# Optimization experiments

Measured on AMD Instinct MI355X. Metric: run time of the kernel, lower is better.

## Reference

```python
import jax, jax.numpy as jnp
import numpy as np

K = 3          # deformable conv kernel size
PAD = 1        # padding
BN_EPS = 1e-5


def _upsample2(x):
    # nn.Upsample(scale_factor=2) default mode='nearest' on [B,C,D,H,W]
    x = jnp.repeat(x, 2, axis=2)
    x = jnp.repeat(x, 2, axis=3)
    x = jnp.repeat(x, 2, axis=4)
    return x


def _conv3d(x, w, b):
    out = jax.lax.conv_general_dilated(
        x, w, window_strides=(1, 1, 1), padding=[(PAD, PAD)] * 3,
        dimension_numbers=('NCDHW', 'OIDHW', 'NCDHW'))
    return out + b[None, :, None, None, None]


def _trilinear_sample(x, coords):
    # x: [B,C,D,H,W]; coords: [B,Kt,3,D,H,W] absolute (possibly OOB) positions.
    # Zero padding outside the volume (standard deformable-conv convention).
    B, C, D, H, W = x.shape
    pd, ph, pw = coords[:, :, 0], coords[:, :, 1], coords[:, :, 2]  # [B,Kt,D,H,W]
    d0 = jnp.floor(pd); h0 = jnp.floor(ph); w0 = jnp.floor(pw)
    fd = pd - d0; fh = ph - h0; fw = pw - w0
    x_flat = x.reshape(B, C, D * H * W)

    def gather(di, hi, wi):
        valid = ((di >= 0) & (di < D) & (hi >= 0) & (hi < H) & (wi >= 0) & (wi < W))
        dc = jnp.clip(di, 0, D - 1).astype(jnp.int32)
        hc = jnp.clip(hi, 0, H - 1).astype(jnp.int32)
        wc = jnp.clip(wi, 0, W - 1).astype(jnp.int32)
        flat = (dc * H + hc) * W + wc                       # [B,Kt,D,H,W]
        vals = jax.vmap(lambda xf, idx: jnp.take(xf, idx.reshape(-1), axis=1))(x_flat, flat)
        vals = vals.reshape(B, C, *flat.shape[1:])          # [B,C,Kt,D,H,W]
        return vals * valid[:, None].astype(x.dtype)

    out = jnp.zeros((B, C) + pd.shape[1:], x.dtype)
    for dd in (0, 1):
        for hh in (0, 1):
            for ww in (0, 1):
                wgt = ((fd if dd else 1.0 - fd)
                       * (fh if hh else 1.0 - fh)
                       * (fw if ww else 1.0 - fw))           # [B,Kt,D,H,W]
                out = out + gather(d0 + dd, h0 + hh, w0 + ww) * wgt[:, None]
    return out  # [B,C,Kt,D,H,W]


def _deform_conv3d(x, w_off, b_off, w, b):
    B, C, D, H, W = x.shape
    Kt = K ** 3
    # offsets: Conv3d(C, 3*K^3, k=3, pad=1) -> [B, Kt, 3(dz,dy,dx), D,H,W]
    off = _conv3d(x, w_off, b_off).reshape(B, Kt, 3, D, H, W)
    # kernel tap displacements relative to output voxel: [Kt,3]
    taps = jnp.stack(jnp.meshgrid(jnp.arange(K), jnp.arange(K), jnp.arange(K),
                                  indexing='ij'), -1).reshape(-1, 3).astype(x.dtype) - PAD
    grid = jnp.stack(jnp.meshgrid(jnp.arange(D, dtype=x.dtype),
                                  jnp.arange(H, dtype=x.dtype),
                                  jnp.arange(W, dtype=x.dtype),
                                  indexing='ij'), 0)          # [3,D,H,W]
    coords = grid[None, None] + taps[None, :, :, None, None, None] + off  # [B,Kt,3,D,H,W]
    sampled = _trilinear_sample(x, coords)                    # [B,C,Kt,D,H,W]
    out = jnp.einsum('bckdhw,ock->bodhw', sampled, w.reshape(w.shape[0], C, Kt))
    return out + b[None, :, None, None, None]


def setup_inputs() -> dict:
    key = jax.random.key(0)
    ks = jax.random.split(key, 4)
    ch_in, ch_out = 64, 32
    x = jax.random.normal(ks[0], (1, ch_in, 16, 16, 16), jnp.float32)
    w_off = jax.random.normal(ks[1], (3 * K ** 3, ch_in, K, K, K), jnp.float32) * 0.01
    b_off = jnp.zeros((3 * K ** 3,), jnp.float32)
    w = jax.random.normal(ks[2], (ch_out, ch_in, K, K, K), jnp.float32) * 0.05
    b = jnp.zeros((ch_out,), jnp.float32)
    gamma = jnp.ones((ch_out,), jnp.float32)
    beta = jnp.zeros((ch_out,), jnp.float32)
    return {"x": x, "w_off": w_off, "b_off": b_off, "w": w, "b": b,
            "gamma": gamma, "beta": beta}


def reference(x, w_off, b_off, w, b, gamma, beta):
    x = _upsample2(x)                                  # [B,C,2D,2H,2W]
    out = _deform_conv3d(x, w_off, b_off, w, b)        # [B,ch_out,2D,2H,2W]
    # BatchNorm3d (training-mode batch stats) + ReLU
    mean = out.mean(axis=(0, 2, 3, 4), keepdims=True)
    var = out.var(axis=(0, 2, 3, 4), keepdims=True)
    out = (out - mean) * jax.lax.rsqrt(var + BN_EPS)
    out = out * gamma[None, :, None, None, None] + beta[None, :, None, None, None]
    return jax.nn.relu(out)
```

## Files before the change

kernel.cpp:

```cpp
#include <hip/hip_runtime.h>
#include <math.h>

#define NVOX  32768
#define CIN   64
#define COUT  32
#define KT    27
#define CIT   1728
#define PSP   5832

#define WS_XT   0
#define WS_WA   186624
#define WS_W2   214272
#define WS_STAT 410880
#define WS_P    410944

typedef __attribute__((ext_vector_type(8))) _Float16 half8;
typedef __attribute__((ext_vector_type(2))) _Float16 half2v;
typedef __attribute__((ext_vector_type(4))) float floatx4;

static __device__ __forceinline__ unsigned dup16(float w) {
    unsigned short b = __builtin_bit_cast(unsigned short, (_Float16)w);
    return (unsigned)b * 0x10001u;
}
static __device__ __forceinline__ half2v u2h2(unsigned u) {
    return __builtin_bit_cast(half2v, u);
}
static __device__ __forceinline__ half8 pk8(half2v a, half2v b, half2v c, half2v d) {
    union { half8 v; half2v p[4]; } u;
    u.p[0] = a; u.p[1] = b; u.p[2] = c; u.p[3] = d;
    return u.v;
}

__global__ __launch_bounds__(256) void prep_all_kernel(
        const float* __restrict__ x, const float* __restrict__ w_off,
        const float* __restrict__ wmat, float* __restrict__ ws) {
    int b = blockIdx.x, t = threadIdx.x;
    if (b < 92) {
        __shared__ _Float16 tile[64][65];
        _Float16* xth = (_Float16*)(ws + WS_XT);
        int tq = t >> 6, lane = t & 63;
        int base = b * 64;
        int cell = base + lane;
        int qw = cell % 18, qh = (cell / 18) % 18, qd = cell / 324;
        bool interior = (cell < PSP) && qd >= 1 && qd <= 16 && qh >= 1 && qh <= 16
                        && qw >= 1 && qw <= 16;
        int xbase = interior ? (((qd - 1) * 16 + (qh - 1)) * 16 + (qw - 1)) : 0;
#pragma unroll
        for (int i = 0; i < 16; i++) {
            int c = tq * 16 + i;
            float v = interior ? x[c * 4096 + xbase] : 0.f;
            tile[lane][c] = (_Float16)v;
        }
        __syncthreads();
#pragma unroll
        for (int i = 0; i < 16; i++) {
            int s = tq * 16 + i;
            int cell2 = base + s;
            if (cell2 < PSP) xth[cell2 * 64 + lane] = tile[s][lane];
        }
    } else if (b < 119) {
        _Float16* wa = (_Float16*)(ws + WS_WA);
        int idx = (b - 92) * 256 + t;
        int kb = idx >> 5, o = idx & 31;
        half8 r;
#pragma unroll
        for (int j = 0; j < 8; j++) {
            int kk = kb * 8 + j;
            int tap = kk >> 6, ci = kk & 63;
            r[j] = (_Float16)wmat[o * CIT + ci * 27 + tap];
        }
        *(half8*)(wa + idx * 8) = r;
    } else if (b < 311) {
        _Float16* w2 = (_Float16*)(ws + WS_W2);
        int idx = (b - 119) * 256 + t;
        int pi = idx / 6144;
        int rem = idx - pi * 6144;
        int kb = rem / 96, m = rem - (rem / 96) * 96;
        int pid = pi >> 2, pih = (pi >> 1) & 1, piw = pi & 1;
        half8 r;
#pragma unroll
        for (int j = 0; j < 8; j++) {
            int kk = kb * 8 + j;
            int tap2 = kk >> 6, ci = kk & 63;
            int cd = tap2 >> 2, ch = (tap2 >> 1) & 1, cw = tap2 & 1;
            int bd = pid ? (cd ? 2 : 0) : cd;
            int nd = pid ? (cd ? 1 : 2) : (cd ? 2 : 1);
            int bh = pih ? (ch ? 2 : 0) : ch;
            int nh = pih ? (ch ? 1 : 2) : (ch ? 2 : 1);
            int bw = piw ? (cw ? 2 : 0) : cw;
            int nw = piw ? (cw ? 1 : 2) : (cw ? 2 : 1);
            float s = 0.f;
            if (m < 81) {
                const float* wp = w_off + (m * 64 + ci) * 27;
                for (int a = 0; a < nd; a++)
                    for (int bb = 0; bb < nh; bb++)
                        for (int c = 0; c < nw; c++)
                            s += wp[(bd + a) * 9 + (bh + bb) * 3 + (bw + c)];
            }
            r[j] = (_Float16)s;
        }
        *(half8*)(w2 + idx * 8) = r;
    } else {
        if (t < 64) ws[WS_STAT + t] = 0.f;
    }
}

__global__ __launch_bounds__(256, 4) void offset_kernel(
        const float* __restrict__ b_off, float* ws) {
    __shared__ __align__(16) _Float16 abuf[2 * 6144];
    int tid = threadIdx.x, wave = tid >> 6, lane = tid & 63;
    int nsub = wave & 1, kh = wave >> 1;
    int col = lane & 15, quad = lane >> 4;
    int bid = blockIdx.x;
    int pi = bid >> 7, tile = bid & 127;
    int pid = pi >> 2, pih = (pi >> 1) & 1, piw = pi & 1;
    int qd = tile >> 3, qh = (tile & 7) * 2 + nsub;
    const char* xtb = (const char*)(ws + WS_XT);
    const int4* wsrc = (const int4*)(ws + WS_W2) + pi * 6144;
    _Float16* Pw = (_Float16*)(ws + WS_P);
    int4* ab4 = (int4*)abuf;

    int4 bx[8];
#pragma unroll
    for (int tap = 0; tap < 8; tap++) {
        int cd = tap >> 2, ch = (tap >> 1) & 1, cw = tap & 1;
        int cell = ((qd + cd + pid) * 18 + (qh + ch + pih)) * 18 + (col + cw + piw);
        bx[tap] = *(const int4*)(xtb + cell * 128 + kh * 64 + quad * 16);
    }

    int4 ra0 = wsrc[tid], ra1 = wsrc[256 + tid], ra2 = wsrc[512 + tid];
    ab4[tid] = ra0; ab4[256 + tid] = ra1; ab4[512 + tid] = ra2;
    ra0 = wsrc[768 + tid]; ra1 = wsrc[768 + 256 + tid]; ra2 = wsrc[768 + 512 + tid];
    __syncthreads();

    floatx4 acc[6];
#pragma unroll
    for (int mt = 0; mt < 6; mt++) acc[mt] = (floatx4){0.f, 0.f, 0.f, 0.f};

    int fb = (kh * 4 + quad) * 768 + col * 8;

#pragma unroll
    for (int tap = 0; tap < 8; tap++) {
        if (tap < 7) {
            int4* dst = ab4 + ((tap + 1) & 1) * 768;
            dst[tid] = ra0; dst[256 + tid] = ra1; dst[512 + tid] = ra2;
        }
        if (tap < 6) {
            const int4* s2 = wsrc + (tap + 2) * 768;
            ra0 = s2[tid]; ra1 = s2[256 + tid]; ra2 = s2[512 + tid];
        }
        half8 bfrag = __builtin_bit_cast(half8, bx[tap]);
        const _Float16* abh = abuf + (tap & 1) * 6144;
#pragma unroll
        for (int mt = 0; mt < 6; mt++) {
            half8 af = *(const half8*)(abh + fb + mt * 128);
            acc[mt] = __builtin_amdgcn_mfma_f32_16x16x32_f16(af, bfrag, acc[mt], 0, 0, 0);
        }
        __syncthreads();
    }

    float* red = (float*)abuf;
    if (kh == 1) {
#pragma unroll
        for (int mt = 0; mt < 6; mt++)
#pragma unroll
            for (int r = 0; r < 4; r++)
                red[(nsub * 96 + mt * 16 + quad * 4 + r) * 17 + col] = acc[mt][r];
    }
    __syncthreads();
    if (kh == 0) {
        int d = 2 * qd + pid, h = 2 * qh + pih;
        int vbase = (d * 32 + h) * 32 + piw;
#pragma unroll
        for (int mt = 0; mt < 6; mt++)
#pragma unroll
            for (int r = 0; r < 4; r++) {
                int m = mt * 16 + quad * 4 + r;
                if (m < 81) {
                    float v = acc[mt][r] + red[(nsub * 96 + m) * 17 + col] + b_off[m];
                    Pw[m * NVOX + vbase + 2 * col] = (_Float16)v;
                }
            }
    }
}

#define ACCP(xl, xh, Wx) do { \
    s00 += (Wx) * u2h2((unsigned)(xl).x); s01 += (Wx) * u2h2((unsigned)(xl).y); \
    s02 += (Wx) * u2h2((unsigned)(xl).z); s03 += (Wx) * u2h2((unsigned)(xl).w); \
    s10 += (Wx) * u2h2((unsigned)(xh).x); s11 += (Wx) * u2h2((unsigned)(xh).y); \
    s12 += (Wx) * u2h2((unsigned)(xh).z); s13 += (Wx) * u2h2((unsigned)(xh).w); \
} while (0)

#define DO2(ap, wp) do { \
    int a0_ = (ap) & 0x7fff, a1_ = (int)((((unsigned)(ap)) >> 16) & 0x7fffu); \
    unsigned wl_ = ((unsigned)(wp) & 0xffffu) * 0x10001u; \
    unsigned wh_ = (((unsigned)(wp)) >> 16) * 0x10001u; \
    int4 x0l_ = *(const int4*)(region + (a0_ ^ subLo)); \
    int4 x0h_ = *(const int4*)(region + (a0_ ^ subHi)); \
    int4 x1l_ = *(const int4*)(region + (a1_ ^ subLo)); \
    int4 x1h_ = *(const int4*)(region + (a1_ ^ subHi)); \
    ACCP(x0l_, x0h_, u2h2(wl_)); ACCP(x1l_, x1h_, u2h2(wh_)); \
} while (0)

#define GSLOW(Ax, wf) do { \
    half2v Wq_ = u2h2(dup16(wf)); \
    int4 xl_ = *(const int4*)(xtb + (Ax) + subLo); \
    int4 xh_ = *(const int4*)(xtb + (Ax) + subLo + 64); \
    t00 += Wq_ * u2h2((unsigned)xl_.x); t01 += Wq_ * u2h2((unsigned)xl_.y); \
    t02 += Wq_ * u2h2((unsigned)xl_.z); t03 += Wq_ * u2h2((unsigned)xl_.w); \
    t10 += Wq_ * u2h2((unsigned)xh_.x); t11 += Wq_ * u2h2((unsigned)xh_.y); \
    t12 += Wq_ * u2h2((unsigned)xh_.z); t13 += Wq_ * u2h2((unsigned)xh_.w); \
} while (0)

__global__ __launch_bounds__(256, 5) void deform_kernel(
        const float* __restrict__ bias, float* ws, float* __restrict__ out) {
    __shared__ __align__(16) char region[25600];
    __shared__ __align__(16) int2 scratch[4][16][6];
    float* pbuf = (float*)region;
    float* rsumS = (float*)(region + 8704);
    float* rsqS  = (float*)(region + 8704 + 128);

    int tid = threadIdx.x, wave = tid >> 6, lane = tid & 63;
    int col = lane & 15, quad = lane >> 4;
    int bid = blockIdx.x;
    int d0 = (bid >> 6) << 1, h0 = ((bid >> 2) & 15) << 1, w0 = (bid & 3) << 3;

    const char* xtb = (const char*)(ws + WS_XT);
    const half8* wa8 = (const half8*)(ws + WS_WA);
    const _Float16* P = (const _Float16*)(ws + WS_P);
    float* gstat = ws + WS_STAT;

    int pdlo = (d0 >> 1) - 1, phlo = (h0 >> 1) - 1, pwlo = (w0 >> 1) - 1;

#pragma unroll 1
    for (int it = 0; it < 7; it++) {
        int i = it * 256 + tid;
        if (i < 1600) {
            int r = i >> 3, c16 = i & 7;
            int rd = r / 40, rem = r - rd * 40, rh = rem >> 3, rw = rem & 7;
            int pd = min(max(pdlo + rd, 0), 17);
            int ph = min(max(phlo + rh, 0), 17);
            int pw = min(max(pwlo + rw, 0), 17);
            int cell = (pd * 18 + ph) * 18 + pw;
            int4 vsrc = *(const int4*)(xtb + cell * 128 + c16 * 16);
            int f = (r ^ (r >> 3)) & 7;
            *(int4*)(region + r * 128 + ((c16 ^ f) << 4)) = vsrc;
        }
    }
    __syncthreads();

    int vh = wave & 1, kt = wave >> 1;
    int v = vh * 16 + col;
    int dv = v >> 4, hv = (v >> 3) & 1, wv = v & 7;
    int dcoord = d0 + dv, hcoord = h0 + hv, wcoord = w0 + wv;
    int gvox = dcoord * 1024 + hcoord * 32 + wcoord;
    int tbeg = kt ? 14 : 0, tend = kt ? 27 : 14;
    int subLo = quad * 16, subHi = subLo + 64;
    int bd = quad >> 1, bh = quad & 1;

    floatx4 acc0 = {0.f, 0.f, 0.f, 0.f}, acc1 = {0.f, 0.f, 0.f, 0.f};

    float od = (float)P[(3 * tbeg + 0) * NVOX + gvox];
    float oh = (float)P[(3 * tbeg + 1) * NVOX + gvox];
    float ow = (float)P[(3 * tbeg + 2) * NVOX + gvox];

#pragma unroll 1
    for (int tap = tbeg; tap < tend; tap++) {
        int kd = tap / 9, r9 = tap - kd * 9, kh2 = r9 / 3, kw2 = r9 - kh2 * 3;
        float pdc = (float)(dcoord + kd - 1) + od;
        float phc = (float)(hcoord + kh2 - 1) + oh;
        float pwc = (float)(wcoord + kw2 - 1) + ow;
        float fd0 = floorf(pdc), fh0 = floorf(phc), fw0 = floorf(pwc);
        float fd = pdc - fd0, fh = phc - fh0, fw = pwc - fw0;
        int id = (int)fd0, ih = (int)fh0, iw = (int)fw0;

        int cd0 = ((min(max(id,     -2), 33)) >> 1) + 1;
        int cd1 = ((min(max(id + 1, -2), 33)) >> 1) + 1;
        int ch0 = ((min(max(ih,     -2), 33)) >> 1) + 1;
        int ch1 = ((min(max(ih + 1, -2), 33)) >> 1) + 1;
        int cw0 = ((min(max(iw,     -2), 33)) >> 1) + 1;
        int cw1 = ((min(max(iw + 1, -2), 33)) >> 1) + 1;
        int sd0 = cd0 - pdlo, sd1 = cd1 - pdlo;
        int sh0 = ch0 - phlo, sh1 = ch1 - phlo;
        int sw0 = cw0 - pwlo, sw1 = cw1 - pwlo;
        bool oob = ((unsigned)sd0 > 4u) | ((unsigned)sd1 > 4u)
                 | ((unsigned)sh0 > 4u) | ((unsigned)sh1 > 4u)
                 | ((unsigned)sw0 > 7u) | ((unsigned)sw1 > 7u);

        int sdq = bd ? sd1 : sd0, shq = bh ? sh1 : sh0;
        int rb = (sdq * 5 + shq) * 8;
        int r0 = rb + sw0, r1 = rb + sw1;
        int f0 = (r0 ^ (r0 >> 3)) & 7, f1 = (r1 ^ (r1 >> 3)) & 7;
        int a0 = oob ? 0x8000 : ((r0 << 7) | (f0 << 4));
        int a1 = oob ? 0x8000 : ((r1 << 7) | (f1 << 4));
        float gdw = 1.f - fd, ghw = 1.f - fh, gww = 1.f - fw;
        float wd = bd ? fd : gdw, wh = bh ? fh : ghw;
        float wdh = wd * wh;
        unsigned wb0 = (unsigned)__builtin_bit_cast(unsigned short, (_Float16)(wdh * gww));
        unsigned wb1 = (unsigned)__builtin_bit_cast(unsigned short, (_Float16)(wdh * fw));
        scratch[wave][col][quad] = make_int2(a0 | (a1 << 16), (int)(wb0 | (wb1 << 16)));

        if (tap + 1 < tend) {
            od = (float)P[(3 * tap + 3) * NVOX + gvox];
            oh = (float)P[(3 * tap + 4) * NVOX + gvox];
            ow = (float)P[(3 * tap + 5) * NVOX + gvox];
        }

        int kb = tap * 8 + quad;
        half8 a00 = wa8[kb * 32 + col];
        half8 a01 = wa8[kb * 32 + 16 + col];
        half8 a10 = wa8[(kb + 4) * 32 + col];
        half8 a11 = wa8[(kb + 4) * 32 + 16 + col];

        const int4* sc = (const int4*)&scratch[wave][col][0];
        int4 p0 = sc[0], p1 = sc[1];

        half2v s00 = {0, 0}, s01 = {0, 0}, s02 = {0, 0}, s03 = {0, 0};
        half2v s10 = {0, 0}, s11 = {0, 0}, s12 = {0, 0}, s13 = {0, 0};
        DO2(p0.x, p0.y); DO2(p0.z, p0.w);
        DO2(p1.x, p1.y); DO2(p1.z, p1.w);

        if (__any((p0.x & 0x8000) != 0)) {
            bool flg = (p0.x & 0x8000) != 0;
            int Rd0 = ((min(max(id,     -2), 33) >> 1) + 1) * (324 * 128);
            int Rd1 = ((min(max(id + 1, -2), 33) >> 1) + 1) * (324 * 128);
            int Rh0 = ((min(max(ih,     -2), 33) >> 1) + 1) * (18 * 128);
            int Rh1 = ((min(max(ih + 1, -2), 33) >> 1) + 1) * (18 * 128);
            int Rw0 = ((min(max(iw,     -2), 33) >> 1) + 1) * 128;
            int Rw1 = ((min(max(iw + 1, -2), 33) >> 1) + 1) * 128;
            half2v t00 = {0,0}, t01 = {0,0}, t02 = {0,0}, t03 = {0,0};
            half2v t10 = {0,0}, t11 = {0,0}, t12 = {0,0}, t13 = {0,0};
            GSLOW(Rd0 + Rh0 + Rw0, gdw * ghw * gww);
            GSLOW(Rd0 + Rh0 + Rw1, gdw * ghw * fw);
            GSLOW(Rd0 + Rh1 + Rw0, gdw * fh  * gww);
            GSLOW(Rd0 + Rh1 + Rw1, gdw * fh  * fw);
            GSLOW(Rd1 + Rh0 + Rw0, fd  * ghw * gww);
            GSLOW(Rd1 + Rh0 + Rw1, fd  * ghw * fw);
            GSLOW(Rd1 + Rh1 + Rw0, fd  * fh  * gww);
            GSLOW(Rd1 + Rh1 + Rw1, fd  * fh  * fw);
            s00 = flg ? t00 : s00; s01 = flg ? t01 : s01;
            s02 = flg ? t02 : s02; s03 = flg ? t03 : s03;
            s10 = flg ? t10 : s10; s11 = flg ? t11 : s11;
            s12 = flg ? t12 : s12; s13 = flg ? t13 : s13;
        }

        half8 bf0 = pk8(s00, s01, s02, s03);
        half8 bf1 = pk8(s10, s11, s12, s13);

        acc0 = __builtin_amdgcn_mfma_f32_16x16x32_f16(a00, bf0, acc0, 0, 0, 0);
        acc1 = __builtin_amdgcn_mfma_f32_16x16x32_f16(a01, bf0, acc1, 0, 0, 0);
        acc0 = __builtin_amdgcn_mfma_f32_16x16x32_f16(a10, bf1, acc0, 0, 0, 0);
        acc1 = __builtin_amdgcn_mfma_f32_16x16x32_f16(a11, bf1, acc1, 0, 0, 0);
    }

    __syncthreads();
    if (kt == 1) {
#pragma unroll
        for (int r = 0; r < 4; r++) {
            pbuf[((vh * 2 + 0) * 16 + quad * 4 + r) * 17 + col] = acc0[r];
            pbuf[((vh * 2 + 1) * 16 + quad * 4 + r) * 17 + col] = acc1[r];
        }
    }
    if (tid < 64) ((float*)(region + 8704))[tid] = 0.f;
    __syncthreads();
    if (kt == 0) {
#pragma unroll
        for (int r = 0; r < 4; r++) {
            int i = quad * 4 + r;
            int o0 = i;
            float v0 = acc0[r] + pbuf[((vh * 2 + 0) * 16 + i) * 17 + col] + bias[o0];
            out[o0 * NVOX + gvox] = v0;
            atomicAdd(&rsumS[o0], v0);
            atomicAdd(&rsqS[o0], v0 * v0);
            int o1 = 16 + i;
            float v1 = acc1[r] + pbuf[((vh * 2 + 1) * 16 + i) * 17 + col] + bias[o1];
            out[o1 * NVOX + gvox] = v1;
            atomicAdd(&rsumS[o1], v1);
            atomicAdd(&rsqS[o1], v1 * v1);
        }
    }
    __syncthreads();
    if (tid < COUT) {
        atomicAdd(&gstat[tid], rsumS[tid]);
        atomicAdd(&gstat[COUT + tid], rsqS[tid]);
    }
}

__global__ void bn_kernel(const float* __restrict__ ws,
                          const float* __restrict__ gamma,
                          const float* __restrict__ beta,
                          float* out) {
    int i = blockIdx.x * 256 + threadIdx.x;
    int o = i >> 15;
    const float* gstat = ws + WS_STAT;
    const float inv = 1.f / 32768.f;
    float mean = gstat[o] * inv;
    float var  = gstat[COUT + o] * inv - mean * mean;
    float sc   = rsqrtf(var + 1e-5f) * gamma[o];
    float v = (out[i] - mean) * sc + beta[o];
    out[i] = fmaxf(v, 0.f);
}

extern "C" void kernel_launch(void* const* d_in, const int* in_sizes, int n_in,
                              void* d_out, int out_size, void* d_ws, size_t ws_size,
                              hipStream_t stream) {
    const float* x     = (const float*)d_in[0];
    const float* w_off = (const float*)d_in[1];
    const float* b_off = (const float*)d_in[2];
    const float* wmat  = (const float*)d_in[3];
    const float* bias  = (const float*)d_in[4];
    const float* gamma = (const float*)d_in[5];
    const float* beta  = (const float*)d_in[6];
    float* ws  = (float*)d_ws;
    float* out = (float*)d_out;

    prep_all_kernel<<<312, 256, 0, stream>>>(x, w_off, wmat, ws);
    offset_kernel<<<1024, 256, 0, stream>>>(b_off, ws);
    deform_kernel<<<1024, 256, 0, stream>>>(bias, ws, out);
    bn_kernel<<<4096, 256, 0, stream>>>(ws, gamma, beta, out);
}
```

Baseline: 140.4 us.

## Fuse offset convolution into deformable kernel with parity-aligned voxel tiles

Merges the offset-prediction MFMA kernel into the deformable sampling kernel. Each block now handles 32 voxels sharing one upsample parity class, and the offsets go to shared memory instead of a global fp16 buffer. This removes a kernel launch and the global write and read of the 81-channel offset tensor. It also shrinks the staged low-res input halo to 4x4x10 cells. In exchange, each block uses more LDS, the occupancy bound drops from 5 to 4, and output writes are strided by parity.

```diff
diff --git a/kernel.cpp b/kernel.cpp
--- a/kernel.cpp
+++ b/kernel.cpp
@@ -12,7 +12,6 @@
 #define WS_WA   186624
 #define WS_W2   214272
 #define WS_STAT 410880
-#define WS_P    410944
 
 typedef __attribute__((ext_vector_type(8))) _Float16 half8;
 typedef __attribute__((ext_vector_type(2))) _Float16 half2v;
@@ -105,85 +104,6 @@
     }
 }
 
-__global__ __launch_bounds__(256, 4) void offset_kernel(
-        const float* __restrict__ b_off, float* ws) {
-    __shared__ __align__(16) _Float16 abuf[2 * 6144];
-    int tid = threadIdx.x, wave = tid >> 6, lane = tid & 63;
-    int nsub = wave & 1, kh = wave >> 1;
-    int col = lane & 15, quad = lane >> 4;
-    int bid = blockIdx.x;
-    int pi = bid >> 7, tile = bid & 127;
-    int pid = pi >> 2, pih = (pi >> 1) & 1, piw = pi & 1;
-    int qd = tile >> 3, qh = (tile & 7) * 2 + nsub;
-    const char* xtb = (const char*)(ws + WS_XT);
-    const int4* wsrc = (const int4*)(ws + WS_W2) + pi * 6144;
-    _Float16* Pw = (_Float16*)(ws + WS_P);
-    int4* ab4 = (int4*)abuf;
-
-    int4 bx[8];
-#pragma unroll
-    for (int tap = 0; tap < 8; tap++) {
-        int cd = tap >> 2, ch = (tap >> 1) & 1, cw = tap & 1;
-        int cell = ((qd + cd + pid) * 18 + (qh + ch + pih)) * 18 + (col + cw + piw);
-        bx[tap] = *(const int4*)(xtb + cell * 128 + kh * 64 + quad * 16);
-    }
-
-    int4 ra0 = wsrc[tid], ra1 = wsrc[256 + tid], ra2 = wsrc[512 + tid];
-    ab4[tid] = ra0; ab4[256 + tid] = ra1; ab4[512 + tid] = ra2;
-    ra0 = wsrc[768 + tid]; ra1 = wsrc[768 + 256 + tid]; ra2 = wsrc[768 + 512 + tid];
-    __syncthreads();
-
-    floatx4 acc[6];
-#pragma unroll
-    for (int mt = 0; mt < 6; mt++) acc[mt] = (floatx4){0.f, 0.f, 0.f, 0.f};
-
-    int fb = (kh * 4 + quad) * 768 + col * 8;
-
-#pragma unroll
-    for (int tap = 0; tap < 8; tap++) {
-        if (tap < 7) {
-            int4* dst = ab4 + ((tap + 1) & 1) * 768;
-            dst[tid] = ra0; dst[256 + tid] = ra1; dst[512 + tid] = ra2;
-        }
-        if (tap < 6) {
-            const int4* s2 = wsrc + (tap + 2) * 768;
-            ra0 = s2[tid]; ra1 = s2[256 + tid]; ra2 = s2[512 + tid];
-        }
-        half8 bfrag = __builtin_bit_cast(half8, bx[tap]);
-        const _Float16* abh = abuf + (tap & 1) * 6144;
-#pragma unroll
-        for (int mt = 0; mt < 6; mt++) {
-            half8 af = *(const half8*)(abh + fb + mt * 128);
-            acc[mt] = __builtin_amdgcn_mfma_f32_16x16x32_f16(af, bfrag, acc[mt], 0, 0, 0);
-        }
-        __syncthreads();
-    }
-
-    float* red = (float*)abuf;
-    if (kh == 1) {
-#pragma unroll
-        for (int mt = 0; mt < 6; mt++)
-#pragma unroll
-            for (int r = 0; r < 4; r++)
-                red[(nsub * 96 + mt * 16 + quad * 4 + r) * 17 + col] = acc[mt][r];
-    }
-    __syncthreads();
-    if (kh == 0) {
-        int d = 2 * qd + pid, h = 2 * qh + pih;
-        int vbase = (d * 32 + h) * 32 + piw;
-#pragma unroll
-        for (int mt = 0; mt < 6; mt++)
-#pragma unroll
-            for (int r = 0; r < 4; r++) {
-                int m = mt * 16 + quad * 4 + r;
-                if (m < 81) {
-                    float v = acc[mt][r] + red[(nsub * 96 + m) * 17 + col] + b_off[m];
-                    Pw[m * NVOX + vbase + 2 * col] = (_Float16)v;
-                }
-            }
-    }
-}
-
 #define ACCP(xl, xh, Wx) do { \
     s00 += (Wx) * u2h2((unsigned)(xl).x); s01 += (Wx) * u2h2((unsigned)(xl).y); \
     s02 += (Wx) * u2h2((unsigned)(xl).z); s03 += (Wx) * u2h2((unsigned)(xl).w); \
@@ -212,47 +132,116 @@
     t12 += Wq_ * u2h2((unsigned)xh_.z); t13 += Wq_ * u2h2((unsigned)xh_.w); \
 } while (0)
 
-__global__ __launch_bounds__(256, 5) void deform_kernel(
-        const float* __restrict__ bias, float* ws, float* __restrict__ out) {
-    __shared__ __align__(16) char region[25600];
-    __shared__ __align__(16) int2 scratch[4][16][6];
-    float* pbuf = (float*)region;
-    float* rsumS = (float*)(region + 8704);
-    float* rsqS  = (float*)(region + 8704 + 128);
+__global__ __launch_bounds__(256, 4) void fused_kernel(
+        const float* __restrict__ b_off, const float* __restrict__ bias,
+        float* ws, float* __restrict__ out) {
+    __shared__ __align__(16) char shmem[30720];
+    char* region = shmem;
+    int2* scratch2 = (int2*)(shmem + 20480);
+    _Float16* Pl = (_Float16*)(shmem + 24576);
+    float* pbuf = (float*)shmem;
+    float* rsumS = (float*)(shmem + 8704);
+    float* rsqS  = (float*)(shmem + 8832);
 
     int tid = threadIdx.x, wave = tid >> 6, lane = tid & 63;
     int col = lane & 15, quad = lane >> 4;
     int bid = blockIdx.x;
-    int d0 = (bid >> 6) << 1, h0 = ((bid >> 2) & 15) << 1, w0 = (bid & 3) << 3;
+    int pi = bid >> 7, tile = bid & 127;
+    int pid = pi >> 2, pih = (pi >> 1) & 1, piw = pi & 1;
+    int qd0 = (tile >> 4) << 1;
+    int qh0 = ((tile >> 1) & 7) << 1;
+    int qw0 = (tile & 1) << 3;
 
     const char* xtb = (const char*)(ws + WS_XT);
     const half8* wa8 = (const half8*)(ws + WS_WA);
-    const _Float16* P = (const _Float16*)(ws + WS_P);
     float* gstat = ws + WS_STAT;
 
-    int pdlo = (d0 >> 1) - 1, phlo = (h0 >> 1) - 1, pwlo = (w0 >> 1) - 1;
+    {
+        int4* ab4 = (int4*)shmem;
+        const _Float16* abuf16 = (const _Float16*)shmem;
+        const int4* wsrc = (const int4*)(ws + WS_W2) + pi * 6144;
+        int nsub = wave & 1, kh = wave >> 1;
+        int vv = nsub * 16 + col;
+        int qdv = qd0 + (vv >> 4), qhv = qh0 + ((vv >> 3) & 1), qwv = qw0 + (vv & 7);
+
+        int4 bx[8];
+#pragma unroll
+        for (int tap = 0; tap < 8; tap++) {
+            int cd = tap >> 2, ch = (tap >> 1) & 1, cw = tap & 1;
+            int cell = ((qdv + cd + pid) * 18 + (qhv + ch + pih)) * 18 + (qwv + cw + piw);
+            bx[tap] = *(const int4*)(xtb + cell * 128 + kh * 64 + quad * 16);
+        }
+
+        int4 ra0 = wsrc[tid], ra1 = wsrc[256 + tid], ra2 = wsrc[512 + tid];
+        ab4[tid] = ra0; ab4[256 + tid] = ra1; ab4[512 + tid] = ra2;
+        ra0 = wsrc[768 + tid]; ra1 = wsrc[768 + 256 + tid]; ra2 = wsrc[768 + 512 + tid];
+        __syncthreads();
+
+        floatx4 acc[6];
+#pragma unroll
+        for (int mt = 0; mt < 6; mt++) acc[mt] = (floatx4){0.f, 0.f, 0.f, 0.f};
+
+        int fb = (kh * 4 + quad) * 768 + col * 8;
+
+#pragma unroll
+        for (int tap = 0; tap < 8; tap++) {
+            if (tap < 7) {
+                int4* dst = ab4 + ((tap + 1) & 1) * 768;
+                dst[tid] = ra0; dst[256 + tid] = ra1; dst[512 + tid] = ra2;
+            }
+            if (tap < 6) {
+                const int4* s2 = wsrc + (tap + 2) * 768;
+                ra0 = s2[tid]; ra1 = s2[256 + tid]; ra2 = s2[512 + tid];
+            }
+            half8 bfrag = __builtin_bit_cast(half8, bx[tap]);
+            const _Float16* abh = abuf16 + (tap & 1) * 6144;
+#pragma unroll
+            for (int mt = 0; mt < 6; mt++) {
+                half8 af = *(const half8*)(abh + fb + mt * 128);
+                acc[mt] = __builtin_amdgcn_mfma_f32_16x16x32_f16(af, bfrag, acc[mt], 0, 0, 0);
+            }
+            __syncthreads();
+        }
+
+        float* red = (float*)shmem;
+        if (kh == 1) {
+#pragma unroll
+            for (int mt = 0; mt < 6; mt++)
+#pragma unroll
+                for (int r = 0; r < 4; r++)
+                    red[(nsub * 96 + mt * 16 + quad * 4 + r) * 17 + col] = acc[mt][r];
+        }
+        __syncthreads();
+        if (kh == 0) {
+#pragma unroll
+            for (int mt = 0; mt < 6; mt++)
+#pragma unroll
+                for (int r = 0; r < 4; r++) {
+                    int m = mt * 16 + quad * 4 + r;
+                    if (m < 81)
+                        Pl[m * 32 + vv] = (_Float16)(acc[mt][r]
+                                         + red[(nsub * 96 + m) * 17 + col] + b_off[m]);
+                }
+        }
+        __syncthreads();
+    }
 
 #pragma unroll 1
-    for (int it = 0; it < 7; it++) {
+    for (int it = 0; it < 5; it++) {
         int i = it * 256 + tid;
-        if (i < 1600) {
-            int r = i >> 3, c16 = i & 7;
-            int rd = r / 40, rem = r - rd * 40, rh = rem >> 3, rw = rem & 7;
-            int pd = min(max(pdlo + rd, 0), 17);
-            int ph = min(max(phlo + rh, 0), 17);
-            int pw = min(max(pwlo + rw, 0), 17);
-            int cell = (pd * 18 + ph) * 18 + pw;
-            int4 vsrc = *(const int4*)(xtb + cell * 128 + c16 * 16);
-            int f = (r ^ (r >> 3)) & 7;
-            *(int4*)(region + r * 128 + ((c16 ^ f) << 4)) = vsrc;
-        }
+        int r = i >> 3, c16 = i & 7;
+        int rd = r / 40, rem = r - rd * 40, rh = rem / 10, rw = rem - rh * 10;
+        int cell = ((qd0 + rd) * 18 + (qh0 + rh)) * 18 + (qw0 + rw);
+        int4 vsrc = *(const int4*)(xtb + cell * 128 + c16 * 16);
+        int f = (r ^ (r >> 3)) & 7;
+        *(int4*)(region + r * 128 + ((c16 ^ f) << 4)) = vsrc;
     }
     __syncthreads();
 
     int vh = wave & 1, kt = wave >> 1;
     int v = vh * 16 + col;
-    int dv = v >> 4, hv = (v >> 3) & 1, wv = v & 7;
-    int dcoord = d0 + dv, hcoord = h0 + hv, wcoord = w0 + wv;
+    int qdv = qd0 + (v >> 4), qhv = qh0 + ((v >> 3) & 1), qwv = qw0 + (v & 7);
+    int dcoord = 2 * qdv + pid, hcoord = 2 * qhv + pih, wcoord = 2 * qwv + piw;
     int gvox = dcoord * 1024 + hcoord * 32 + wcoord;
     int tbeg = kt ? 14 : 0, tend = kt ? 27 : 14;
     int subLo = quad * 16, subHi = subLo + 64;
@@ -260,9 +249,9 @@
 
     floatx4 acc0 = {0.f, 0.f, 0.f, 0.f}, acc1 = {0.f, 0.f, 0.f, 0.f};
 
-    float od = (float)P[(3 * tbeg + 0) * NVOX + gvox];
-    float oh = (float)P[(3 * tbeg + 1) * NVOX + gvox];
-    float ow = (float)P[(3 * tbeg + 2) * NVOX + gvox];
+    float od = (float)Pl[(3 * tbeg + 0) * 32 + v];
+    float oh = (float)Pl[(3 * tbeg + 1) * 32 + v];
+    float ow = (float)Pl[(3 * tbeg + 2) * 32 + v];
 
 #pragma unroll 1
     for (int tap = tbeg; tap < tend; tap++) {
@@ -280,15 +269,15 @@
         int ch1 = ((min(max(ih + 1, -2), 33)) >> 1) + 1;
         int cw0 = ((min(max(iw,     -2), 33)) >> 1) + 1;
         int cw1 = ((min(max(iw + 1, -2), 33)) >> 1) + 1;
-        int sd0 = cd0 - pdlo, sd1 = cd1 - pdlo;
-        int sh0 = ch0 - phlo, sh1 = ch1 - phlo;
-        int sw0 = cw0 - pwlo, sw1 = cw1 - pwlo;
-        bool oob = ((unsigned)sd0 > 4u) | ((unsigned)sd1 > 4u)
-                 | ((unsigned)sh0 > 4u) | ((unsigned)sh1 > 4u)
-                 | ((unsigned)sw0 > 7u) | ((unsigned)sw1 > 7u);
+        int sd0 = cd0 - qd0, sd1 = cd1 - qd0;
+        int sh0 = ch0 - qh0, sh1 = ch1 - qh0;
+        int sw0 = cw0 - qw0, sw1 = cw1 - qw0;
+        bool oob = ((unsigned)sd0 > 3u) | ((unsigned)sd1 > 3u)
+                 | ((unsigned)sh0 > 3u) | ((unsigned)sh1 > 3u)
+                 | ((unsigned)sw0 > 9u) | ((unsigned)sw1 > 9u);
 
         int sdq = bd ? sd1 : sd0, shq = bh ? sh1 : sh0;
-        int rb = (sdq * 5 + shq) * 8;
+        int rb = (sdq * 4 + shq) * 10;
         int r0 = rb + sw0, r1 = rb + sw1;
         int f0 = (r0 ^ (r0 >> 3)) & 7, f1 = (r1 ^ (r1 >> 3)) & 7;
         int a0 = oob ? 0x8000 : ((r0 << 7) | (f0 << 4));
@@ -298,12 +287,13 @@
         float wdh = wd * wh;
         unsigned wb0 = (unsigned)__builtin_bit_cast(unsigned short, (_Float16)(wdh * gww));
         unsigned wb1 = (unsigned)__builtin_bit_cast(unsigned short, (_Float16)(wdh * fw));
-        scratch[wave][col][quad] = make_int2(a0 | (a1 << 16), (int)(wb0 | (wb1 << 16)));
+        scratch2[(wave * 16 + col) * 6 + quad] =
+            make_int2(a0 | (a1 << 16), (int)(wb0 | (wb1 << 16)));
 
         if (tap + 1 < tend) {
-            od = (float)P[(3 * tap + 3) * NVOX + gvox];
-            oh = (float)P[(3 * tap + 4) * NVOX + gvox];
-            ow = (float)P[(3 * tap + 5) * NVOX + gvox];
+            od = (float)Pl[(3 * tap + 3) * 32 + v];
+            oh = (float)Pl[(3 * tap + 4) * 32 + v];
+            ow = (float)Pl[(3 * tap + 5) * 32 + v];
         }
 
         int kb = tap * 8 + quad;
@@ -312,7 +302,7 @@
         half8 a10 = wa8[(kb + 4) * 32 + col];
         half8 a11 = wa8[(kb + 4) * 32 + 16 + col];
 
-        const int4* sc = (const int4*)&scratch[wave][col][0];
+        const int4* sc = (const int4*)(scratch2 + (wave * 16 + col) * 6);
         int4 p0 = sc[0], p1 = sc[1];
 
         half2v s00 = {0, 0}, s01 = {0, 0}, s02 = {0, 0}, s03 = {0, 0};
@@ -361,7 +351,7 @@
             pbuf[((vh * 2 + 1) * 16 + quad * 4 + r) * 17 + col] = acc1[r];
         }
     }
-    if (tid < 64) ((float*)(region + 8704))[tid] = 0.f;
+    if (tid < 64) ((float*)(shmem + 8704))[tid] = 0.f;
     __syncthreads();
     if (kt == 0) {
 #pragma unroll
@@ -415,7 +405,6 @@
     float* out = (float*)d_out;
 
     prep_all_kernel<<<312, 256, 0, stream>>>(x, w_off, wmat, ws);
-    offset_kernel<<<1024, 256, 0, stream>>>(b_off, ws);
-    deform_kernel<<<1024, 256, 0, stream>>>(bias, ws, out);
+    fused_kernel<<<1024, 256, 0, stream>>>(b_off, bias, ws, out);
     bn_kernel<<<4096, 256, 0, stream>>>(ws, gamma, beta, out);
 }
```

Result: faster. 134.5 us (-4.2%).
